# Optimization experiments

Hardware: AMD Instinct MI355X
Metric: run time of the kernel (lower is better)

Reference implementation:

```python
import jax, jax.numpy as jnp
import numpy as np

D = 1024
H = 16
DH = D // H


def setup_inputs() -> dict:
    key = jax.random.key(0)
    ks = jax.random.split(key, 10)
    B, S = 2, 2048
    scale = 1.0 / np.sqrt(D)
    inp = {
        "hidden_states": jax.random.normal(ks[0], (B, S, D), dtype=jnp.float32),
        "attention_mask": jnp.ones((B * H, 1, S), dtype=bool),
        "W_q": jax.random.normal(ks[1], (D, D), dtype=jnp.float32) * scale,
        "b_q": jnp.zeros((D,), dtype=jnp.float32),
        "W_k": jax.random.normal(ks[2], (D, D), dtype=jnp.float32) * scale,
        "b_k": jnp.zeros((D,), dtype=jnp.float32),
        "W_v": jax.random.normal(ks[3], (D, D), dtype=jnp.float32) * scale,
        "b_v": jnp.zeros((D,), dtype=jnp.float32),
        "W_o": jax.random.normal(ks[4], (D, D), dtype=jnp.float32) * scale,
        "b_o": jnp.zeros((D,), dtype=jnp.float32),
    }
    return inp


def _split_heads(x):
    # [B, S, D] -> [B*H, S, DH]
    B, S, _ = x.shape
    return x.reshape(B, S, H, DH).transpose(0, 2, 1, 3).reshape(B * H, S, DH)


def _merge_heads(x, B):
    # [B*H, S, DH] -> [B, S, D]
    S = x.shape[1]
    return x.reshape(B, H, S, DH).transpose(0, 2, 1, 3).reshape(B, S, D)


def reference(hidden_states, attention_mask, W_q, b_q, W_k, b_k, W_v, b_v, W_o, b_o):
    B = hidden_states.shape[0]
    q = _split_heads(hidden_states @ W_q + b_q)
    k = _split_heads(hidden_states @ W_k + b_k)
    v = _split_heads(hidden_states @ W_v + b_v)
    # naive full attention: materialize [B*H, S, S] scores, as in the source
    dots = jnp.einsum("bqd,bkd->bqk", q, k) / jnp.sqrt(jnp.float32(DH))
    dots = jnp.where(attention_mask, dots, jnp.float32(-1e9))
    # logsumexp-normalized softmax, exactly as the torch code
    probs = jnp.exp(dots - jax.nn.logsumexp(dots, axis=-1, keepdims=True))
    attn = jnp.einsum("bqk,bkd->bqd", probs, v)
    out = _merge_heads(attn, B)
    return out @ W_o + b_o
```

## Files before the change

### kernel.cpp

```cpp
#include <hip/hip_runtime.h>

typedef unsigned short u16;
typedef unsigned int u32;
typedef __attribute__((ext_vector_type(8))) u16 u16x8;
typedef __attribute__((ext_vector_type(4))) u16 u16x4;
typedef __attribute__((ext_vector_type(8))) __bf16 v8bf;
typedef __attribute__((ext_vector_type(4))) short s16x4;
typedef __attribute__((ext_vector_type(4))) float f32x4;

static __device__ __forceinline__ u16 f2b(float f) {
    u32 u = __float_as_uint(f);
    return (u16)((u + 0x7FFFu + ((u >> 16) & 1u)) >> 16);
}
static __device__ __forceinline__ float b2f(u16 x) { return __uint_as_float(((u32)x) << 16); }
static __device__ __forceinline__ v8bf asbf(u16x8 v) { return __builtin_bit_cast(v8bf, v); }

static __device__ __forceinline__ f32x4 mfma16(u16x4 a, u16x4 b, f32x4 c) {
#if defined(__HIP_DEVICE_COMPILE__)
#if __has_builtin(__builtin_amdgcn_mfma_f32_16x16x16bf16_1k)
    return __builtin_amdgcn_mfma_f32_16x16x16bf16_1k(
        __builtin_bit_cast(s16x4, a), __builtin_bit_cast(s16x4, b), c, 0, 0, 0);
#else
    f32x4 d;
    asm("v_mfma_f32_16x16x16_bf16 %0, %1, %2, %3"
        : "=v"(d) : "v"(a), "v"(b), "v"(c));
    return d;
#endif
#else
    (void)a; (void)b; return c;
#endif
}

static __device__ __forceinline__ float fexp2(float x) {
#if defined(__HIP_DEVICE_COMPILE__)
#if __has_builtin(__builtin_amdgcn_exp2f)
    return __builtin_amdgcn_exp2f(x);
#else
    return exp2f(x);
#endif
#else
    return x;
#endif
}

static __device__ __forceinline__ void gl_lds16(const u16* g, u16* l) {
    __builtin_amdgcn_global_load_lds(
        (const __attribute__((address_space(1))) u32*)g,
        (__attribute__((address_space(3))) u32*)l, 16, 0, 0);
}

__global__ void detect_dtype(const u32* __restrict__ X, int* __restrict__ flag)
{
    int lane = threadIdx.x;
    int c = 0;
    for (int j = 0; j < 4; ++j) {
        u32 u = X[lane * 4 + j];
        int e = (u >> 7) & 0xFF;
        c += (e >= 100 && e <= 129) ? 1 : 0;
    }
    for (int m = 1; m < 64; m <<= 1) c += __shfl_xor(c, m, 64);
    if (lane == 0) *flag = (c < 192) ? 1 : 0;
}

__global__ __launch_bounds__(256) void convert_bf16(
    const void* __restrict__ src, u16* __restrict__ dst, int n,
    const int* __restrict__ flagp)
{
    int isf = *flagp;
    int i = blockIdx.x * 256 + threadIdx.x;
    if (i * 8 >= n) return;
    int base = i * 8;
    u16x8 o;
    if (isf) {
        const float* s = (const float*)src + base;
        for (int j = 0; j < 8; ++j) o[j] = f2b(s[j]);
    } else {
        o = *(const u16x8*)((const u16*)src + base);
    }
    *(u16x8*)(dst + base) = o;
}

__global__ __launch_bounds__(256) void transpose4(
    const void* __restrict__ W0, const void* __restrict__ W1,
    const void* __restrict__ W2, const void* __restrict__ W3,
    u16* __restrict__ Wtf, u16* __restrict__ Wto,
    const int* __restrict__ flagp)
{
    __shared__ __align__(16) u16 tile[64][72];
    int isf = *flagp;
    int z = blockIdx.z;
    const void* W = (z == 0) ? W0 : (z == 1) ? W1 : (z == 2) ? W2 : W3;
    u16* T = (z < 3) ? (Wtf + (size_t)z * 1024 * 1024) : Wto;
    int kb = blockIdx.y * 64, nb = blockIdx.x * 64;
    int t = threadIdx.x;
    int r = t >> 2, c = (t & 3) * 16;
    size_t off = (size_t)(kb + r) * 1024 + nb + c;
    if (isf) {
        const float* s = (const float*)W + off;
        for (int j = 0; j < 16; ++j) tile[r][c + j] = f2b(s[j]);
    } else {
        const u16* s = (const u16*)W + off;
        *(u16x8*)&tile[r][c] = *(const u16x8*)s;
        *(u16x8*)&tile[r][c + 8] = *(const u16x8*)(s + 8);
    }
    __syncthreads();
    u16x8 o0, o1;
    for (int j = 0; j < 8; ++j) { o0[j] = tile[c + j][r]; o1[j] = tile[c + 8 + j][r]; }
    u16* dst = T + (size_t)(nb + r) * 1024 + kb + c;
    *(u16x8*)dst = o0;
    *(u16x8*)(dst + 8) = o1;
}

__global__ __launch_bounds__(256) void gemm_bias(
    const u16* __restrict__ A, const u16* __restrict__ Bt,
    const void* __restrict__ bias0, const void* __restrict__ bias1,
    const void* __restrict__ bias2,
    u16* __restrict__ D0, u16* __restrict__ D1, u16* __restrict__ D2,
    const int* __restrict__ flagp, int mode)
{
    __shared__ __align__(16) u16 As[64 * 64];
    __shared__ __align__(16) u16 Bs[128 * 64];
    const int K = 1024;
    int isf = *flagp;
    int t = threadIdx.x;
    int w = t >> 6, lane = t & 63, quad = lane >> 4, l16 = lane & 15;
    int wr = (w >> 1) * 32, wc = (w & 1) * 64;
    int bm = blockIdx.y * 64, bn = blockIdx.x * 128;
    int r8 = lane >> 3, c8 = lane & 7;
    f32x4 acc[2][4] = {};
    const u16* Ab = A + (size_t)bm * K;
    const u16* Bb = Bt + (size_t)bn * K;
    for (int kb = 0; kb < K; kb += 64) {
        __syncthreads();
        for (int s = 0; s < 2; ++s) {
            int base = w * 16 + s * 8;
            int row = base + r8;
            gl_lds16(Ab + (size_t)row * K + kb + ((c8 ^ (row & 7)) * 8), &As[base * 64]);
        }
        for (int s = 0; s < 4; ++s) {
            int base = w * 32 + s * 8;
            int row = base + r8;
            gl_lds16(Bb + (size_t)row * K + kb + ((c8 ^ (row & 7)) * 8), &Bs[base * 64]);
        }
        __syncthreads();
        v8bf af[2][2], bfb[4][2];
        for (int mt = 0; mt < 2; ++mt) {
            int row = wr + mt * 16 + l16;
            for (int ks = 0; ks < 2; ++ks)
                af[mt][ks] = asbf(*(const u16x8*)&As[row * 64 + (((ks * 4 + quad) ^ (row & 7)) * 8)]);
        }
        for (int nt = 0; nt < 4; ++nt) {
            int row = wc + nt * 16 + l16;
            for (int ks = 0; ks < 2; ++ks)
                bfb[nt][ks] = asbf(*(const u16x8*)&Bs[row * 64 + (((ks * 4 + quad) ^ (row & 7)) * 8)]);
        }
        for (int ks = 0; ks < 2; ++ks)
            for (int mt = 0; mt < 2; ++mt)
                for (int nt = 0; nt < 4; ++nt)
                    acc[mt][nt] = __builtin_amdgcn_mfma_f32_16x16x32_bf16(af[mt][ks], bfb[nt][ks], acc[mt][nt], 0, 0, 0);
    }
    int mid = (bn + wc) >> 10;
    const void* bp = (mid == 0) ? bias0 : (mid == 1) ? bias1 : bias2;
    for (int nt = 0; nt < 4; ++nt) {
        int c = bn + wc + nt * 16 + l16;
        int nn = c & 1023;
        float bsv = isf ? ((const float*)bp)[nn] : b2f(((const u16*)bp)[nn]);
        for (int mt = 0; mt < 2; ++mt) {
            int row0 = bm + wr + mt * 16 + quad * 4;
            if (mode == 0) {
                if (mid == 2) {
                    u16x4 pk;
                    for (int i = 0; i < 4; ++i) pk[i] = f2b(acc[mt][nt][i] + bsv);
                    int bb = row0 >> 11, s = row0 & 2047;
                    int h = nn >> 6, d = nn & 63;
                    *(u16x4*)&D2[(size_t)((bb * 16 + h) * 64 + d) * 2048 + s] = pk;
                } else {
                    u16* dst = (mid == 0) ? D0 : D1;
                    float scl = (mid == 0) ? 0.18033688011112042f : 1.0f;
                    for (int i = 0; i < 4; ++i)
                        dst[(size_t)(row0 + i) * 1024 + nn] = f2b((acc[mt][nt][i] + bsv) * scl);
                }
            } else if (isf) {
                for (int i = 0; i < 4; ++i)
                    ((float*)D0)[(size_t)(row0 + i) * 1024 + nn] = acc[mt][nt][i] + bsv;
            } else {
                for (int i = 0; i < 4; ++i)
                    D0[(size_t)(row0 + i) * 1024 + nn] = f2b(acc[mt][nt][i] + bsv);
            }
        }
    }
}

__global__ __launch_bounds__(256, 2) void attn_kernel(
    const u16* __restrict__ Q, const u16* __restrict__ Kg,
    const u16* __restrict__ Vt, u16* __restrict__ ctx)
{
    __shared__ __align__(16) u16 Ks[2][64 * 64];
    __shared__ __align__(16) u16 Vs[2][64 * 64];
    int t = threadIdx.x;
    int w = t >> 6, lane = t & 63, quad = lane >> 4, l16 = lane & 15;
    int head = blockIdx.x & 31, qt = blockIdx.x >> 5;
    int b = head >> 4, h = head & 15;
    int qbase = qt * 128 + w * 32;
    v8bf bq[2][2];
    for (int mi = 0; mi < 2; ++mi) {
        const u16* qp = Q + (size_t)(b * 2048 + qbase + mi * 16 + l16) * 1024 + h * 64 + quad * 8;
        bq[mi][0] = asbf(*(const u16x8*)qp);
        bq[mi][1] = asbf(*(const u16x8*)(qp + 32));
    }
    f32x4 oaccT[2][4] = {};
    f32x4 oaccDen[2] = {};
    const u16x4 ones = {0x3F80, 0x3F80, 0x3F80, 0x3F80};
    int swl = l16 & 7;
    int kp0[4], kp1[4], vp[4][4];
    for (int nt = 0; nt < 4; ++nt) {
        int row = nt * 16 + l16;
        kp0[nt] = row * 64 + ((quad ^ swl) * 8);
        kp1[nt] = row * 64 + (((quad + 4) ^ swl) * 8);
    }
    for (int dt = 0; dt < 4; ++dt)
        for (int nt = 0; nt < 4; ++nt) {
            int row = dt * 16 + l16;
            int blk = nt * 2 + (quad >> 1);
            vp[dt][nt] = row * 64 + ((blk ^ swl) * 8) + (quad & 1) * 4;
        }
    int srow = t >> 3, spb = t & 7;
    int r0 = srow, r1 = srow + 32;
    const u16* kg0 = Kg + (size_t)(b * 2048 + r0) * 1024 + h * 64 + (spb ^ (r0 & 7)) * 8;
    const u16* kg1 = Kg + (size_t)(b * 2048 + r1) * 1024 + h * 64 + (spb ^ (r1 & 7)) * 8;
    const u16* vg0 = Vt + (size_t)((b * 16 + h) * 64 + r0) * 2048 + (spb ^ (r0 & 7)) * 8;
    const u16* vg1 = Vt + (size_t)((b * 16 + h) * 64 + r1) * 2048 + (spb ^ (r1 & 7)) * 8;
    int wo = w * 512;

    auto stage = [&](int buf) {
        gl_lds16(kg0, &Ks[buf][wo]);
        gl_lds16(kg1, &Ks[buf][2048 + wo]);
        gl_lds16(vg0, &Vs[buf][wo]);
        gl_lds16(vg1, &Vs[buf][2048 + wo]);
        kg0 += 64 * 1024; kg1 += 64 * 1024; vg0 += 64; vg1 += 64;
    };
    auto compute = [&](int buf) {
        f32x4 sc[2][4] = {};
        for (int nt = 0; nt < 4; ++nt) {
            v8bf ak0 = asbf(*(const u16x8*)&Ks[buf][kp0[nt]]);
            v8bf ak1 = asbf(*(const u16x8*)&Ks[buf][kp1[nt]]);
            for (int mi = 0; mi < 2; ++mi) {
                sc[mi][nt] = __builtin_amdgcn_mfma_f32_16x16x32_bf16(ak0, bq[mi][0], sc[mi][nt], 0, 0, 0);
                sc[mi][nt] = __builtin_amdgcn_mfma_f32_16x16x32_bf16(ak1, bq[mi][1], sc[mi][nt], 0, 0, 0);
            }
        }
        for (int nt = 0; nt < 4; ++nt) {
            u16x4 pb[2];
            for (int mi = 0; mi < 2; ++mi)
                for (int i = 0; i < 4; ++i)
                    pb[mi][i] = __builtin_bit_cast(u16, (__bf16)fexp2(sc[mi][nt][i]));
            for (int dt = 0; dt < 4; ++dt) {
                u16x4 av = *(const u16x4*)&Vs[buf][vp[dt][nt]];
                for (int mi = 0; mi < 2; ++mi)
                    oaccT[mi][dt] = mfma16(av, pb[mi], oaccT[mi][dt]);
            }
            for (int mi = 0; mi < 2; ++mi)
                oaccDen[mi] = mfma16(ones, pb[mi], oaccDen[mi]);
        }
    };

    stage(0);
    for (int kt = 0; kt < 2048; kt += 128) {
        __syncthreads();
        if (kt + 64 < 2048) stage(1);
        compute(0);
        __syncthreads();
        if (kt + 128 < 2048) stage(0);
        compute(1);
    }
    float rden[2];
    for (int mi = 0; mi < 2; ++mi) rden[mi] = 1.0f / oaccDen[mi][0];
    for (int mi = 0; mi < 2; ++mi)
        for (int dt = 0; dt < 4; ++dt) {
            u16x4 pk;
            for (int i = 0; i < 4; ++i) pk[i] = f2b(oaccT[mi][dt][i] * rden[mi]);
            int q = qbase + mi * 16 + l16;
            *(u16x4*)&ctx[(size_t)(b * 2048 + q) * 1024 + h * 64 + dt * 16 + quad * 4] = pk;
        }
}

extern "C" void kernel_launch(void* const* d_in, const int* in_sizes, int n_in,
                              void* d_out, int out_size, void* d_ws, size_t ws_size,
                              hipStream_t stream)
{
    const void* X = nullptr;
    const void* W[4] = {nullptr, nullptr, nullptr, nullptr};
    const void* Bb[4] = {nullptr, nullptr, nullptr, nullptr};
    int wi = 0, bi = 0;
    for (int i = 0; i < n_in; ++i) {
        int s = in_sizes[i];
        if (s == 4194304 && !X) X = d_in[i];
        else if (s == 1048576 && wi < 4) W[wi++] = d_in[i];
        else if (s == 1024 && bi < 4) Bb[bi++] = d_in[i];
    }
    if (!X) X = d_in[0];
    if (wi < 4) { W[0] = d_in[2]; W[1] = d_in[4]; W[2] = d_in[6]; W[3] = d_in[8]; }
    if (bi < 4) { Bb[0] = d_in[3]; Bb[1] = d_in[5]; Bb[2] = d_in[7]; Bb[3] = d_in[9]; }

    u16* ws = (u16*)d_ws;
    int* flag = (int*)d_ws;
    const size_t WSZ = 1024u * 1024u;
    const size_t BSZ = 4096u * 1024u;
    u16* Wtf = ws + 32;
    u16* Wto = Wtf + 3 * WSZ;
    u16* Xb  = Wto + WSZ;
    u16* Kb  = Xb + BSZ;
    u16* Vtb = Kb + BSZ;
    u16* Cb  = Xb;
    u16* Qb  = (u16*)d_out;

    detect_dtype<<<1, 64, 0, stream>>>((const u32*)X, flag);
    convert_bf16<<<2048, 256, 0, stream>>>(X, Xb, 4194304, flag);
    transpose4<<<dim3(16, 16, 4), 256, 0, stream>>>(W[0], W[1], W[2], W[3], Wtf, Wto, flag);
    gemm_bias<<<dim3(24, 64), 256, 0, stream>>>(Xb, Wtf, Bb[0], Bb[1], Bb[2],
                                                Qb, Kb, Vtb, flag, 0);
    attn_kernel<<<512, 256, 0, stream>>>(Qb, Kb, Vtb, Cb);
    gemm_bias<<<dim3(8, 64), 256, 0, stream>>>(Cb, Wto, Bb[3], nullptr, nullptr,
                                               (u16*)d_out, nullptr, nullptr, flag, 1);
}
```

Measured before the change: 212.1 us.

## Use 16x16x32 bf16 MFMA for PV product via permuted key-row staging

Switches the P·V and denominator products from 16x16x16 MFMAs to 16x16x32 MFMAs, merging two key sub-tiles per instruction. To make the score accumulator layout match the wider B operand, K rows are loaded into LDS in a permuted order (keyrow), and V reads become 8-element vector loads. This halves the PV MFMA instruction count and LDS read operations, and adds explicit unroll pragmas. It depends on the row permutation matching the MFMA register layout exactly.

Measured after the change: 206.4 us. 2.7% less time.

```diff
diff --git a/kernel.cpp b/kernel.cpp
--- a/kernel.cpp
+++ b/kernel.cpp
@@ -14,22 +14,6 @@
 }
 static __device__ __forceinline__ float b2f(u16 x) { return __uint_as_float(((u32)x) << 16); }
 static __device__ __forceinline__ v8bf asbf(u16x8 v) { return __builtin_bit_cast(v8bf, v); }
-
-static __device__ __forceinline__ f32x4 mfma16(u16x4 a, u16x4 b, f32x4 c) {
-#if defined(__HIP_DEVICE_COMPILE__)
-#if __has_builtin(__builtin_amdgcn_mfma_f32_16x16x16bf16_1k)
-    return __builtin_amdgcn_mfma_f32_16x16x16bf16_1k(
-        __builtin_bit_cast(s16x4, a), __builtin_bit_cast(s16x4, b), c, 0, 0, 0);
-#else
-    f32x4 d;
-    asm("v_mfma_f32_16x16x16_bf16 %0, %1, %2, %3"
-        : "=v"(d) : "v"(a), "v"(b), "v"(c));
-    return d;
-#endif
-#else
-    (void)a; (void)b; return c;
-#endif
-}
 
 static __device__ __forceinline__ float fexp2(float x) {
 #if defined(__HIP_DEVICE_COMPILE__)
@@ -47,6 +31,10 @@
     __builtin_amdgcn_global_load_lds(
         (const __attribute__((address_space(1))) u32*)g,
         (__attribute__((address_space(3))) u32*)l, 16, 0, 0);
+}
+
+static __device__ __forceinline__ int keyrow(int r) {
+    return (r & ~31) | ((r & 12) << 1) | ((r & 16) >> 2) | (r & 3);
 }
 
 __global__ void detect_dtype(const u32* __restrict__ X, int* __restrict__ flag)
@@ -210,24 +198,25 @@
     }
     f32x4 oaccT[2][4] = {};
     f32x4 oaccDen[2] = {};
-    const u16x4 ones = {0x3F80, 0x3F80, 0x3F80, 0x3F80};
+    const u16x8 onesb = {0x3F80, 0x3F80, 0x3F80, 0x3F80, 0x3F80, 0x3F80, 0x3F80, 0x3F80};
+    const v8bf onesv = asbf(onesb);
     int swl = l16 & 7;
-    int kp0[4], kp1[4], vp[4][4];
+    int kp0[4], kp1[4], vp[4][2];
     for (int nt = 0; nt < 4; ++nt) {
         int row = nt * 16 + l16;
         kp0[nt] = row * 64 + ((quad ^ swl) * 8);
         kp1[nt] = row * 64 + (((quad + 4) ^ swl) * 8);
     }
     for (int dt = 0; dt < 4; ++dt)
-        for (int nt = 0; nt < 4; ++nt) {
+        for (int p = 0; p < 2; ++p) {
             int row = dt * 16 + l16;
-            int blk = nt * 2 + (quad >> 1);
-            vp[dt][nt] = row * 64 + ((blk ^ swl) * 8) + (quad & 1) * 4;
+            vp[dt][p] = row * 64 + (((p * 4 + quad) ^ swl) * 8);
         }
     int srow = t >> 3, spb = t & 7;
     int r0 = srow, r1 = srow + 32;
-    const u16* kg0 = Kg + (size_t)(b * 2048 + r0) * 1024 + h * 64 + (spb ^ (r0 & 7)) * 8;
-    const u16* kg1 = Kg + (size_t)(b * 2048 + r1) * 1024 + h * 64 + (spb ^ (r1 & 7)) * 8;
+    int k0 = keyrow(r0), k1 = keyrow(r1);
+    const u16* kg0 = Kg + (size_t)(b * 2048 + k0) * 1024 + h * 64 + (spb ^ (r0 & 7)) * 8;
+    const u16* kg1 = Kg + (size_t)(b * 2048 + k1) * 1024 + h * 64 + (spb ^ (r1 & 7)) * 8;
     const u16* vg0 = Vt + (size_t)((b * 16 + h) * 64 + r0) * 2048 + (spb ^ (r0 & 7)) * 8;
     const u16* vg1 = Vt + (size_t)((b * 16 + h) * 64 + r1) * 2048 + (spb ^ (r1 & 7)) * 8;
     int wo = w * 512;
@@ -241,26 +230,37 @@
     };
     auto compute = [&](int buf) {
         f32x4 sc[2][4] = {};
+#pragma unroll
         for (int nt = 0; nt < 4; ++nt) {
             v8bf ak0 = asbf(*(const u16x8*)&Ks[buf][kp0[nt]]);
             v8bf ak1 = asbf(*(const u16x8*)&Ks[buf][kp1[nt]]);
+#pragma unroll
             for (int mi = 0; mi < 2; ++mi) {
                 sc[mi][nt] = __builtin_amdgcn_mfma_f32_16x16x32_bf16(ak0, bq[mi][0], sc[mi][nt], 0, 0, 0);
                 sc[mi][nt] = __builtin_amdgcn_mfma_f32_16x16x32_bf16(ak1, bq[mi][1], sc[mi][nt], 0, 0, 0);
             }
         }
-        for (int nt = 0; nt < 4; ++nt) {
-            u16x4 pb[2];
+#pragma unroll
+        for (int p = 0; p < 2; ++p) {
+            u16x8 pb[2];
+#pragma unroll
             for (int mi = 0; mi < 2; ++mi)
-                for (int i = 0; i < 4; ++i)
-                    pb[mi][i] = __builtin_bit_cast(u16, (__bf16)fexp2(sc[mi][nt][i]));
+#pragma unroll
+                for (int hi = 0; hi < 2; ++hi)
+#pragma unroll
+                    for (int i = 0; i < 4; ++i)
+                        pb[mi][hi * 4 + i] =
+                            __builtin_bit_cast(u16, (__bf16)fexp2(sc[mi][2 * p + hi][i]));
+#pragma unroll
             for (int dt = 0; dt < 4; ++dt) {
-                u16x4 av = *(const u16x4*)&Vs[buf][vp[dt][nt]];
+                v8bf av = asbf(*(const u16x8*)&Vs[buf][vp[dt][p]]);
+#pragma unroll
                 for (int mi = 0; mi < 2; ++mi)
-                    oaccT[mi][dt] = mfma16(av, pb[mi], oaccT[mi][dt]);
+                    oaccT[mi][dt] = __builtin_amdgcn_mfma_f32_16x16x32_bf16(av, asbf(pb[mi]), oaccT[mi][dt], 0, 0, 0);
             }
+#pragma unroll
             for (int mi = 0; mi < 2; ++mi)
-                oaccDen[mi] = mfma16(ones, pb[mi], oaccDen[mi]);
+                oaccDen[mi] = __builtin_amdgcn_mfma_f32_16x16x32_bf16(onesv, asbf(pb[mi]), oaccDen[mi], 0, 0, 0);
         }
     };
 
```
